# Kernel tuning notes

Hardware: AMD Instinct MI355X
Metric: run time of the kernel (lower is better)

Reference implementation:

```python
import jax, jax.numpy as jnp
import numpy as np

LR = 0.001      # L_r
GAMMA = 0.99    # forgetting factor
LEN_C = 512     # control filter length
R, S, E, T = 4, 8, 8, 2048


def setup_inputs() -> dict:
    key = jax.random.key(0)
    k1, k2, k3, k4 = jax.random.split(key, 4)
    Fx = jax.random.normal(k1, (R, S, E, LEN_C), dtype=jnp.float32)
    Dis = jax.random.normal(k2, (E, LEN_C), dtype=jnp.float32)
    Fx_extend = jax.random.normal(k3, (T, R, S, E, LEN_C), dtype=jnp.float32)
    initial_weights = jax.random.normal(k4, (R, S, LEN_C), dtype=jnp.float32) * 0.01
    return {"Fx": Fx, "Dis": Dis, "Fx_extend": Fx_extend, "initial_weights": initial_weights}


def reference(Fx, Dis, Fx_extend, initial_weights):
    # --- First_grad: closed-form LMS gradient (identical to autograd of sum(error^2)) ---
    # anti_noise[e] = sum_{r,s,n} Fx[r,s,e,n] * W0[r,s,n]
    anti = jnp.einsum('rsen,rsn->e', Fx, initial_weights)          # [E]
    error = Dis[:, -1] - anti                                       # [E]
    # dLoss/dW0[r,s,n] = -2 * sum_e error[e] * Fx[r,s,e,n]
    w_grad = -2.0 * jnp.einsum('e,rsen->rsn', error, Fx)            # [R,S,LEN_C]
    control_weights = initial_weights - 0.5 * LR * w_grad           # [R,S,LEN_C]
    # --- Adaptive_filtering over the full duration ---
    # fuse '...rsen,...rsn->...rse' followed by '...rse->...e' into one einsum
    anti_noise_matrix = jnp.einsum('trsen,rsn->te', Fx_extend, control_weights)  # [T,E]
    # --- Gamma vector: gamma^(LEN_C-1-i) ---
    gam_vector = jnp.power(jnp.float32(GAMMA), (LEN_C - 1) - jnp.arange(LEN_C, dtype=jnp.float32))
    return anti_noise_matrix, gam_vector
```

## Files before the change

kernel.cpp:

```cpp
#include <hip/hip_runtime.h>
#include <hip/hip_bf16.h>

#define LEN_C 512
#define R_DIM 4
#define S_DIM 8
#define E_DIM 8
#define T_DIM 2048
#define Q_DIM (R_DIM * S_DIM)
#define W_ELEMS (Q_DIM * LEN_C)
#define PER_T (Q_DIM * E_DIM * LEN_C)
#define LR_CONST 0.001f

__global__ __launch_bounds__(256) void grad_kernel(
    const float* __restrict__ Fx, const float* __restrict__ Dis,
    const float* __restrict__ W0, float* __restrict__ err) {
  __shared__ float lds[4 * 8];
  float p[E_DIM];
#pragma unroll
  for (int e = 0; e < E_DIM; ++e) p[e] = 0.0f;

  for (int idx = threadIdx.x; idx < W_ELEMS; idx += 256) {
    const int q = idx >> 9;
    const int n = idx & (LEN_C - 1);
    const float w = W0[idx];
    const float* f = Fx + ((size_t)q * E_DIM) * LEN_C + n;
#pragma unroll
    for (int e = 0; e < E_DIM; ++e) p[e] += f[e * LEN_C] * w;
  }

  const int lane = threadIdx.x & 63;
  const int wave = threadIdx.x >> 6;
#pragma unroll
  for (int e = 0; e < E_DIM; ++e) {
    float v = p[e];
    for (int off = 32; off; off >>= 1) v += __shfl_down(v, off, 64);
    if (lane == 0) lds[wave * 8 + e] = v;
  }
  __syncthreads();
  if (threadIdx.x < E_DIM) {
    const float anti = lds[threadIdx.x] + lds[8 + threadIdx.x] +
                       lds[16 + threadIdx.x] + lds[24 + threadIdx.x];
    err[threadIdx.x] = Dis[threadIdx.x * LEN_C + (LEN_C - 1)] - anti;
  }
}

__global__ __launch_bounds__(256) void cw_kernel(
    const float* __restrict__ Fx, const float* __restrict__ W0,
    const float* __restrict__ err, float* __restrict__ cw) {
  const int idx = blockIdx.x * 256 + threadIdx.x;
  const int q = idx >> 9;
  const int n = idx & (LEN_C - 1);
  const float* f = Fx + ((size_t)q * E_DIM) * LEN_C + n;
  float s = 0.0f;
#pragma unroll
  for (int e = 0; e < E_DIM; ++e) s += err[e] * f[e * LEN_C];
  cw[idx] = W0[idx] + LR_CONST * s;
}

__global__ __launch_bounds__(256) void adapt_kernel(
    const float* __restrict__ fxe, const float* __restrict__ cw,
    float* __restrict__ out) {
  const int t = blockIdx.x;
  const int lane = threadIdx.x & 63;
  const int wave = threadIdx.x >> 6;
  const float* base = fxe + (size_t)t * PER_T;

  float acc[E_DIM];
#pragma unroll
  for (int e = 0; e < E_DIM; ++e) acc[e] = 0.0f;

  float4 cwa[8], cwb[8];
#pragma unroll
  for (int i = 0; i < 8; ++i) {
    const int q = wave + 4 * i;
    const float4* c = (const float4*)(cw + q * LEN_C);
    cwa[i] = c[lane];
    cwb[i] = c[lane + 64];
  }

#pragma unroll
  for (int i = 0; i < 8; ++i) {
    const int q = wave + 4 * i;
    const float4* fb = (const float4*)(base + (size_t)q * (E_DIM * LEN_C));
#pragma unroll
    for (int e = 0; e < E_DIM; ++e) {
      const float4 fa = fb[e * 128 + lane];
      const float4 fc = fb[e * 128 + lane + 64];
      acc[e] += fa.x * cwa[i].x + fa.y * cwa[i].y + fa.z * cwa[i].z +
                fa.w * cwa[i].w + fc.x * cwb[i].x + fc.y * cwb[i].y +
                fc.z * cwb[i].z + fc.w * cwb[i].w;
    }
  }

  __shared__ float lds[4 * 8];
#pragma unroll
  for (int e = 0; e < E_DIM; ++e) {
    float v = acc[e];
    for (int off = 32; off; off >>= 1) v += __shfl_down(v, off, 64);
    if (lane == 0) lds[wave * 8 + e] = v;
  }
  __syncthreads();
  if (threadIdx.x < E_DIM) {
    out[(size_t)t * E_DIM + threadIdx.x] =
        lds[threadIdx.x] + lds[8 + threadIdx.x] + lds[16 + threadIdx.x] +
        lds[24 + threadIdx.x];
  }
}

__global__ void gam_kernel(float* __restrict__ out) {
  const int i = threadIdx.x;
  out[T_DIM * E_DIM + i] = powf(0.99f, (float)(LEN_C - 1 - i));
}

extern "C" void kernel_launch(void* const* d_in, const int* in_sizes, int n_in,
                              void* d_out, int out_size, void* d_ws,
                              size_t ws_size, hipStream_t stream) {
  const float* Fx = (const float*)d_in[0];
  const float* Dis = (const float*)d_in[1];
  const float* Fxe = (const float*)d_in[2];
  const float* W0 = (const float*)d_in[3];
  float* out = (float*)d_out;

  float* err = (float*)d_ws;
  float* cw = (float*)((char*)d_ws + 64);

  grad_kernel<<<1, 256, 0, stream>>>(Fx, Dis, W0, err);
  cw_kernel<<<W_ELEMS / 256, 256, 0, stream>>>(Fx, W0, err, cw);
  adapt_kernel<<<T_DIM, 256, 0, stream>>>(Fxe, cw, out);
  gam_kernel<<<1, LEN_C, 0, stream>>>(out);
}
```

Baseline: 1.395 ms.

## Parallelize gradient reduction across blocks and load control weights per iteration

The single-block gradient kernel becomes 32 blocks, one per (r,s) pair, each writing partial per-error sums. The final reduction and error computation move into the start of cw_kernel, where each block recomputes the error into shared memory. In adapt_kernel the 16 preloaded float4 weight registers are replaced by per-iteration loads, and the launch bounds request 4 waves per SIMD to raise occupancy. The error reduction is now done redundantly in every cw block, and the weight loads are no longer hoisted ahead of the main loop.

```diff
diff --git a/kernel.cpp b/kernel.cpp
--- a/kernel.cpp
+++ b/kernel.cpp
@@ -1,5 +1,4 @@
 #include <hip/hip_runtime.h>
-#include <hip/hip_bf16.h>
 
 #define LEN_C 512
 #define R_DIM 4
@@ -12,83 +11,84 @@
 #define LR_CONST 0.001f
 
 __global__ __launch_bounds__(256) void grad_kernel(
-    const float* __restrict__ Fx, const float* __restrict__ Dis,
-    const float* __restrict__ W0, float* __restrict__ err) {
-  __shared__ float lds[4 * 8];
-  float p[E_DIM];
+    const float* __restrict__ Fx, const float* __restrict__ W0,
+    float* __restrict__ partial) {
+  const int q = blockIdx.x;
+  const int lane = threadIdx.x & 63;
+  const int wave = threadIdx.x >> 6;
+
+  const float4* c = (const float4*)(W0 + (size_t)q * LEN_C);
+  const float4 w0 = c[lane];
+  const float4 w1 = c[lane + 64];
+  const float4* fb = (const float4*)(Fx + (size_t)q * (E_DIM * LEN_C));
+
+  float acc[2];
 #pragma unroll
-  for (int e = 0; e < E_DIM; ++e) p[e] = 0.0f;
-
-  for (int idx = threadIdx.x; idx < W_ELEMS; idx += 256) {
-    const int q = idx >> 9;
-    const int n = idx & (LEN_C - 1);
-    const float w = W0[idx];
-    const float* f = Fx + ((size_t)q * E_DIM) * LEN_C + n;
-#pragma unroll
-    for (int e = 0; e < E_DIM; ++e) p[e] += f[e * LEN_C] * w;
+  for (int j = 0; j < 2; ++j) {
+    const int e = wave * 2 + j;
+    const float4 fa = fb[e * 128 + lane];
+    const float4 fc = fb[e * 128 + lane + 64];
+    acc[j] = fa.x * w0.x + fa.y * w0.y + fa.z * w0.z + fa.w * w0.w +
+             fc.x * w1.x + fc.y * w1.y + fc.z * w1.z + fc.w * w1.w;
   }
 
-  const int lane = threadIdx.x & 63;
-  const int wave = threadIdx.x >> 6;
 #pragma unroll
-  for (int e = 0; e < E_DIM; ++e) {
-    float v = p[e];
+  for (int j = 0; j < 2; ++j) {
+    float v = acc[j];
     for (int off = 32; off; off >>= 1) v += __shfl_down(v, off, 64);
-    if (lane == 0) lds[wave * 8 + e] = v;
-  }
-  __syncthreads();
-  if (threadIdx.x < E_DIM) {
-    const float anti = lds[threadIdx.x] + lds[8 + threadIdx.x] +
-                       lds[16 + threadIdx.x] + lds[24 + threadIdx.x];
-    err[threadIdx.x] = Dis[threadIdx.x * LEN_C + (LEN_C - 1)] - anti;
+    if (lane == 0) partial[q * E_DIM + wave * 2 + j] = v;
   }
 }
 
 __global__ __launch_bounds__(256) void cw_kernel(
-    const float* __restrict__ Fx, const float* __restrict__ W0,
-    const float* __restrict__ err, float* __restrict__ cw) {
+    const float* __restrict__ Fx, const float* __restrict__ Dis,
+    const float* __restrict__ partial, const float* __restrict__ W0,
+    float* __restrict__ cw) {
+  __shared__ float serr[E_DIM];
+  if (threadIdx.x < E_DIM) {
+    float s = 0.0f;
+#pragma unroll
+    for (int qq = 0; qq < Q_DIM; ++qq) s += partial[qq * E_DIM + threadIdx.x];
+    serr[threadIdx.x] = Dis[threadIdx.x * LEN_C + (LEN_C - 1)] - s;
+  }
+  __syncthreads();
+
   const int idx = blockIdx.x * 256 + threadIdx.x;
   const int q = idx >> 9;
   const int n = idx & (LEN_C - 1);
   const float* f = Fx + ((size_t)q * E_DIM) * LEN_C + n;
   float s = 0.0f;
 #pragma unroll
-  for (int e = 0; e < E_DIM; ++e) s += err[e] * f[e * LEN_C];
+  for (int e = 0; e < E_DIM; ++e) s += serr[e] * f[e * LEN_C];
   cw[idx] = W0[idx] + LR_CONST * s;
 }
 
-__global__ __launch_bounds__(256) void adapt_kernel(
+__global__ __launch_bounds__(256, 4) void adapt_kernel(
     const float* __restrict__ fxe, const float* __restrict__ cw,
     float* __restrict__ out) {
   const int t = blockIdx.x;
   const int lane = threadIdx.x & 63;
   const int wave = threadIdx.x >> 6;
-  const float* base = fxe + (size_t)t * PER_T;
+  const float4* __restrict__ base =
+      (const float4*)(fxe + (size_t)t * PER_T) + (size_t)wave * (E_DIM * 128);
 
   float acc[E_DIM];
 #pragma unroll
   for (int e = 0; e < E_DIM; ++e) acc[e] = 0.0f;
 
-  float4 cwa[8], cwb[8];
 #pragma unroll
   for (int i = 0; i < 8; ++i) {
     const int q = wave + 4 * i;
-    const float4* c = (const float4*)(cw + q * LEN_C);
-    cwa[i] = c[lane];
-    cwb[i] = c[lane + 64];
-  }
-
-#pragma unroll
-  for (int i = 0; i < 8; ++i) {
-    const int q = wave + 4 * i;
-    const float4* fb = (const float4*)(base + (size_t)q * (E_DIM * LEN_C));
+    const float4* c = (const float4*)(cw + (size_t)q * LEN_C);
+    const float4 w0 = c[lane];
+    const float4 w1 = c[lane + 64];
+    const float4* fb = base + (size_t)i * (4 * E_DIM * 128);
 #pragma unroll
     for (int e = 0; e < E_DIM; ++e) {
       const float4 fa = fb[e * 128 + lane];
       const float4 fc = fb[e * 128 + lane + 64];
-      acc[e] += fa.x * cwa[i].x + fa.y * cwa[i].y + fa.z * cwa[i].z +
-                fa.w * cwa[i].w + fc.x * cwb[i].x + fc.y * cwb[i].y +
-                fc.z * cwb[i].z + fc.w * cwb[i].w;
+      acc[e] += fa.x * w0.x + fa.y * w0.y + fa.z * w0.z + fa.w * w0.w +
+                fc.x * w1.x + fc.y * w1.y + fc.z * w1.z + fc.w * w1.w;
     }
   }
 
@@ -121,11 +121,11 @@
   const float* W0 = (const float*)d_in[3];
   float* out = (float*)d_out;
 
-  float* err = (float*)d_ws;
-  float* cw = (float*)((char*)d_ws + 64);
+  float* partial = (float*)d_ws;
+  float* cw = (float*)((char*)d_ws + 1024);
 
-  grad_kernel<<<1, 256, 0, stream>>>(Fx, Dis, W0, err);
-  cw_kernel<<<W_ELEMS / 256, 256, 0, stream>>>(Fx, W0, err, cw);
+  grad_kernel<<<Q_DIM, 256, 0, stream>>>(Fx, W0, partial);
+  cw_kernel<<<W_ELEMS / 256, 256, 0, stream>>>(Fx, Dis, partial, W0, cw);
   adapt_kernel<<<T_DIM, 256, 0, stream>>>(Fxe, cw, out);
   gam_kernel<<<1, LEN_C, 0, stream>>>(out);
 }
```

Result: slower. 1.717 ms (+23.1%).
